# Kernel optimization log

Measured on AMD Instinct MI355X. Metric: run time of the kernel, lower is better.

Reference implementation:

```python
import jax, jax.numpy as jnp
import numpy as np
import math

LOG2PI = math.log(2.0 * math.pi)

def _silu(x):
    return x * jax.nn.sigmoid(x)

def _gru(x, W_ih, W_hh, b_ih, b_hh):
    # x: [B,T,X]; torch nn.GRU single layer, batch_first
    B = x.shape[0]
    H = W_hh.shape[1]
    gi_all = jnp.einsum('btx,gx->btg', x, W_ih) + b_ih  # [B,T,3H] input gates precomputed
    def step(h, gi):
        gh = h @ W_hh.T + b_hh
        i_r, i_z, i_n = jnp.split(gi, 3, axis=-1)
        h_r, h_z, h_n = jnp.split(gh, 3, axis=-1)
        r = jax.nn.sigmoid(i_r + h_r)
        z = jax.nn.sigmoid(i_z + h_z)
        n = jnp.tanh(i_n + r * h_n)
        h_new = (1.0 - z) * n + z * h
        return h_new, h_new
    h0 = jnp.zeros((B, H), x.dtype)
    h_last, h_seq = jax.lax.scan(step, h0, jnp.swapaxes(gi_all, 0, 1))
    return jnp.swapaxes(h_seq, 0, 1), h_last  # [B,T,H], [B,H]

def _A_Q(kappa, sigma, dt):
    A = jnp.exp(-kappa * dt)
    two_k_dt = 2.0 * kappa * dt
    small = (two_k_dt < 1e-6).astype(dt.dtype)
    Q_exact = sigma ** 2 * (1.0 - jnp.exp(-two_k_dt)) / jnp.maximum(2.0 * kappa, 1e-12)
    Q_taylor = sigma ** 2 * dt * (1.0 - kappa * dt + two_k_dt ** 2 / 6.0)
    Q = small * Q_taylor + (1.0 - small) * Q_exact
    return A, Q

def _ou_posterior(m0, s0, mu_k, A_k, Q_k, eps0, eps):
    B, Tm1, C = mu_k.shape
    c0 = m0 + s0 * eps0  # [B,C]
    s0c = jnp.maximum(s0, 1e-12)
    log_q0 = -0.5 * (((c0 - m0) / s0c) ** 2 + 2.0 * jnp.log(s0c) + LOG2PI).sum(-1)
    noise = eps * jnp.sqrt(jnp.maximum(Q_k, 1e-12))
    b = (1.0 - A_k) * mu_k + noise
    Phi_prefix = jnp.cumprod(A_k, axis=1)  # [B,T-1,C]
    Phi_full = jnp.concatenate([jnp.ones((B, 1, C), mu_k.dtype), Phi_prefix], axis=1)
    denom = jnp.maximum(Phi_full[:, 1:, :], 1e-20)
    s = b / denom
    S_full = jnp.concatenate([jnp.zeros((B, 1, C), mu_k.dtype), jnp.cumsum(s, axis=1)], axis=1)
    c = Phi_full * (c0[:, None, :] + S_full)  # [B,T,C]
    mean_trans = mu_k + A_k * (c[:, :-1, :] - mu_k)
    var_trans = jnp.maximum(Q_k, 1e-12)
    log_q_trans = -0.5 * ((c[:, 1:, :] - mean_trans) ** 2 / var_trans + jnp.log(var_trans) + LOG2PI)
    log_q = log_q0 + log_q_trans.sum(-1).sum(-1)
    return c, log_q

def reference(x, t, eps0, eps, W_ih, W_hh, b_ih, b_hh, Wi1, bi1, Wi2, bi2, Ws1, bs1, Ws2, bs2, Ws3, bs3):
    B, T, _ = x.shape
    h_seq, h_global = _gru(x, W_ih, W_hh, b_ih, b_hh)
    # soft time attention, temperature = 1.0
    delta = t[:, :, None, 0] - t[:, None, :, 0]  # [B,T,T]
    logits = -(T * delta) ** 2  # / tau^2 with tau=1
    w = jax.nn.softmax(logits, axis=-1)
    attn = jnp.einsum('bkj,bjh->bkh', w, h_seq)
    # init head
    h0_ctx = h_global + attn[:, 0, :]
    hi = _silu(h0_ctx @ Wi1.T + bi1)
    m0, logs0 = jnp.split(hi @ Wi2.T + bi2, 2, axis=-1)
    s0 = jax.nn.softplus(logs0) + 1e-6
    # step head on ctx[:, :-1]
    ctx = jnp.concatenate([h_global[:, None, :] + attn, t], axis=-1)[:, :-1, :]
    hs = _silu(ctx @ Ws1.T + bs1)
    hs = _silu(hs @ Ws2.T + bs2)
    params = hs @ Ws3.T + bs3
    mu_k, logk_k, logs_k = jnp.split(params, 3, axis=-1)
    kappa_k = jax.nn.softplus(logk_k) + 1e-6
    sigma_k = jax.nn.softplus(logs_k) + 1e-6
    dt = jnp.maximum(t[:, 1:, :] - t[:, :-1, :], 1e-6)
    A_k, Q_k = _A_Q(kappa_k, sigma_k, dt)
    c, log_q = _ou_posterior(m0, s0, mu_k, A_k, Q_k, eps0, eps)
    return c, log_q

def setup_inputs() -> dict:
    B, T, X, H, C = 8, 2048, 64, 256, 32
    key = jax.random.key(0)
    ks = jax.random.split(key, 16)
    def w(k, shape, scale=0.02):
        return (scale * jax.random.normal(k, shape)).astype(jnp.float32)
    x = jax.random.normal(ks[0], (B, T, X), dtype=jnp.float32)
    t = jnp.sort(jax.random.uniform(ks[1], (B, T, 1), dtype=jnp.float32), axis=1)
    eps0 = jax.random.normal(ks[2], (B, C), dtype=jnp.float32)
    eps = jax.random.normal(ks[3], (B, T - 1, C), dtype=jnp.float32)
    return {
        'x': x, 't': t, 'eps0': eps0, 'eps': eps,
        'W_ih': w(ks[4], (3 * H, X)), 'W_hh': w(ks[5], (3 * H, H)),
        'b_ih': jnp.zeros((3 * H,), jnp.float32), 'b_hh': jnp.zeros((3 * H,), jnp.float32),
        'Wi1': w(ks[6], (H, H)), 'bi1': jnp.zeros((H,), jnp.float32),
        'Wi2': w(ks[7], (2 * C, H)), 'bi2': jnp.zeros((2 * C,), jnp.float32),
        'Ws1': w(ks[8], (H, H + 1)), 'bs1': jnp.zeros((H,), jnp.float32),
        'Ws2': w(ks[9], (H, H)), 'bs2': jnp.zeros((H,), jnp.float32),
        'Ws3': w(ks[10], (3 * C, H)), 'bs3': jnp.zeros((3 * C,), jnp.float32),
    }
```

## Files before the change

### kernel.cpp

```cpp
#include <hip/hip_runtime.h>
#include <hip/hip_fp16.h>

#define LOG2PI_F 1.8378770664093453f

typedef float f32x4 __attribute__((ext_vector_type(4)));
typedef unsigned int u32x4 __attribute__((ext_vector_type(4)));

__device__ __forceinline__ unsigned int packh2(float lo, float hi) {
  unsigned int l = (unsigned int)__half_as_ushort(__float2half(lo));
  unsigned int h = (unsigned int)__half_as_ushort(__float2half(hi));
  return (h << 16) | l;
}

__device__ __forceinline__ float sigmoid_f(float x) { return 1.f / (1.f + __expf(-x)); }
__device__ __forceinline__ float silu_f(float x) { return x * sigmoid_f(x); }
__device__ __forceinline__ float softplus_f(float x) {
  return fmaxf(x, 0.f) + log1pf(__expf(-fabsf(x)));
}
__device__ __forceinline__ float tanh_f(float x) {
  float ax = fabsf(x);
  float e = __expf(2.f * ax);
  return copysignf(1.f - 2.f / (e + 1.f), x);
}

__device__ __forceinline__ void tr_piece(const float* in, float* out, int R, int C,
                                         int i) {
  if (i < R * C) {
    int r = i / C, c = i % C;
    out[c * R + r] = in[i];
  }
}

__global__ void prep_kernel(const float* W_ih, const float* Wi1, const float* Wi2,
                            const float* Ws1, const float* Ws2, const float* Ws3,
                            const float* W_hh, float* WT_ih, float* WT1, float* WT2,
                            float* WTs1, float* WTs2, float* WTs3,
                            unsigned int* Wrow) {
  int blk = blockIdx.x;
  int tid = threadIdx.x;
  if (blk < 192) {
    tr_piece(W_ih, WT_ih, 768, 64, blk * 256 + tid);
  } else if (blk < 448) {
    tr_piece(Wi1, WT1, 256, 256, (blk - 192) * 256 + tid);
  } else if (blk < 512) {
    tr_piece(Wi2, WT2, 64, 256, (blk - 448) * 256 + tid);
  } else if (blk < 769) {
    tr_piece(Ws1, WTs1, 256, 257, (blk - 512) * 256 + tid);
  } else if (blk < 1025) {
    tr_piece(Ws2, WTs2, 256, 256, (blk - 769) * 256 + tid);
  } else if (blk < 1121) {
    tr_piece(Ws3, WTs3, 96, 256, (blk - 1025) * 256 + tid);
  } else {
    int i = (blk - 1121) * 256 + tid;
    if (i < 98304) {
      int r = i >> 7, kp = i & 127;
      Wrow[i] = packh2(W_hh[r * 256 + 2 * kp], W_hh[r * 256 + 2 * kp + 1]);
    }
  }
}

__global__ void gi_gemm(const float* __restrict__ x, const float* __restrict__ WT,
                        const float* __restrict__ bih, float* __restrict__ gi) {
  int m0 = blockIdx.x * 8;
  int g = threadIdx.x;
  __shared__ float xs[8][64];
  for (int i = g; i < 512; i += 256) xs[i >> 6][i & 63] = x[m0 * 64 + i];
  __syncthreads();
  float b0 = bih[g], b1 = bih[g + 256], b2 = bih[g + 512];
  float a0[8], a1[8], a2[8];
#pragma unroll
  for (int r = 0; r < 8; r++) { a0[r] = b0; a1[r] = b1; a2[r] = b2; }
  for (int k = 0; k < 64; k++) {
    const float* w = WT + k * 768;
    float w0 = w[g], w1 = w[g + 256], w2 = w[g + 512];
#pragma unroll
    for (int r = 0; r < 8; r++) {
      float xv = xs[r][k];
      a0[r] = fmaf(w0, xv, a0[r]);
      a1[r] = fmaf(w1, xv, a1[r]);
      a2[r] = fmaf(w2, xv, a2[r]);
    }
  }
#pragma unroll
  for (int r = 0; r < 8; r++) {
    float* o = gi + (m0 + r) * 768;
    o[g] = a0[r];
    o[g + 256] = a1[r];
    o[g + 512] = a2[r];
  }
}

__global__ __launch_bounds__(512, 2) void gru_kernel(
    const unsigned int* __restrict__ Wrow,
    const float* __restrict__ gi,
    const float* __restrict__ bhh,
    float* __restrict__ h_seq)
{
  const int b = blockIdx.x;
  const int tid = threadIdx.x;
  const int lane = tid & 63;
  const int wave = tid >> 6;
  const int quad = lane >> 4;
  const int m16 = lane & 15;

  u32x4 afr[6][8];
#pragma unroll
  for (int mt = 0; mt < 6; mt++) {
    int r = wave * 96 + mt * 16 + m16;
    const u32x4* src = (const u32x4*)(Wrow + r * 128);
#pragma unroll
    for (int kt = 0; kt < 8; kt++) afr[mt][kt] = src[kt * 4 + quad];
  }
#pragma unroll
  for (int mt = 0; mt < 6; mt++)
#pragma unroll
    for (int kt = 0; kt < 8; kt++) asm("" : "+a"(afr[mt][kt]));

  __shared__ __align__(16) unsigned int hpk[2][128];
  __shared__ __align__(16) float als[768];
  if (tid < 128) hpk[0][tid] = 0u;

  float brb = 0.f, bzb = 0.f, bnb = 0.f, gr = 0.f, gz = 0.f, gn = 0.f;
  float h = 0.f;
  const float* gib = gi + b * 2048 * 768;
  float* hsb = h_seq + b * 2048 * 256;
  if (tid < 256) {
    brb = bhh[tid];
    bzb = bhh[256 + tid];
    bnb = bhh[512 + tid];
    gr = gib[tid];
    gz = gib[256 + tid];
    gn = gib[512 + tid];
  }
  __syncthreads();

  for (int t = 0; t < 2048; t++) {
    float grn = 0.f, gzn = 0.f, gnn = 0.f;
    if (tid < 256) {
      const float* g3 = gib + min(t + 1, 2047) * 768;
      grn = g3[tid];
      gzn = g3[256 + tid];
      gnn = g3[512 + tid];
    }

    f32x4 c[6];
#pragma unroll
    for (int mt = 0; mt < 6; mt++) c[mt] = (f32x4)0.0f;
    const u32x4* hp = (const u32x4*)hpk[t & 1];
#pragma unroll
    for (int kt = 0; kt < 8; kt++) {
      u32x4 bv = (u32x4)0u;
      if (m16 == 0) bv = hp[kt * 4 + quad];
#pragma unroll
      for (int mt = 0; mt < 6; mt++)
        asm("v_mfma_f32_16x16x32_f16 %0, %1, %2, %0"
            : "+v"(c[mt])
            : "a"(afr[mt][kt]), "v"(bv));
    }
    __builtin_amdgcn_sched_barrier(0);
    asm volatile("s_nop 7\n\ts_nop 7");
    __builtin_amdgcn_sched_barrier(0);

    if (m16 == 0) {
#pragma unroll
      for (int mt = 0; mt < 6; mt++)
        *(f32x4*)(als + wave * 96 + mt * 16 + quad * 4) = c[mt];
    }
    __syncthreads();

    if (tid < 256) {
      float rv = sigmoid_f(als[tid] + brb + gr);
      float zv = sigmoid_f(als[256 + tid] + bzb + gz);
      float nv = tanh_f(gn + rv * (als[512 + tid] + bnb));
      float hn = (1.f - zv) * nv + zv * h;
      h = hn;
      hsb[t * 256 + tid] = hn;
      float other = __shfl_xor(hn, 1);
      if ((tid & 1) == 0) hpk[(t + 1) & 1][tid >> 1] = packh2(hn, other);
    }
    gr = grn;
    gz = gzn;
    gn = gnn;
    __syncthreads();
  }
}

#define AW 80
__global__ void attn_kernel(const float* __restrict__ h_seq, const float* __restrict__ t,
                            float* __restrict__ ctx) {
  const int blk = blockIdx.x;
  const int b = blk >> 7;
  const int k0 = (blk & 127) << 4;
  const int tid = threadIdx.x;

  __shared__ __align__(16) float ewT[176][16];
  __shared__ float ts[176];
  __shared__ float tks[16];
  __shared__ float rden[16];

  const float* tb = t + b * 2048;
  if (tid < 176) {
    int j = k0 - AW + tid;
    ts[tid] = tb[min(max(j, 0), 2047)];
  }
  if (tid < 16) tks[tid] = tb[k0 + tid];
  __syncthreads();

  for (int p = tid; p < 176 * 16; p += 256) {
    int kk = p & 15, jr = p >> 4;
    int j = k0 - AW + jr;
    float d = 2048.f * (tks[kk] - ts[jr]);
    float e = (j >= 0 && j < 2048) ? __expf(-d * d) : 0.f;
    ewT[jr][kk] = e;
  }
  __syncthreads();

  if (tid < 16) {
    float s = 0.f;
    for (int jr = 0; jr < 176; jr++) s += ewT[jr][tid];
    rden[tid] = 1.f / s;
  }
  __syncthreads();

  float acc[16];
#pragma unroll
  for (int kk = 0; kk < 16; kk++) acc[kk] = 0.f;

  const float* hb = h_seq + b * 2048 * 256;
  for (int jr = 0; jr < 176; jr++) {
    int j = min(max(k0 - AW + jr, 0), 2047);
    float hv = hb[j * 256 + tid];
    const float4* e4 = (const float4*)ewT[jr];
    float4 e0 = e4[0], e1 = e4[1], e2 = e4[2], e3 = e4[3];
    acc[0] = fmaf(e0.x, hv, acc[0]);   acc[1] = fmaf(e0.y, hv, acc[1]);
    acc[2] = fmaf(e0.z, hv, acc[2]);   acc[3] = fmaf(e0.w, hv, acc[3]);
    acc[4] = fmaf(e1.x, hv, acc[4]);   acc[5] = fmaf(e1.y, hv, acc[5]);
    acc[6] = fmaf(e1.z, hv, acc[6]);   acc[7] = fmaf(e1.w, hv, acc[7]);
    acc[8] = fmaf(e2.x, hv, acc[8]);   acc[9] = fmaf(e2.y, hv, acc[9]);
    acc[10] = fmaf(e2.z, hv, acc[10]); acc[11] = fmaf(e2.w, hv, acc[11]);
    acc[12] = fmaf(e3.x, hv, acc[12]); acc[13] = fmaf(e3.y, hv, acc[13]);
    acc[14] = fmaf(e3.z, hv, acc[14]); acc[15] = fmaf(e3.w, hv, acc[15]);
  }

  float hg = hb[2047 * 256 + tid];
  float* cb = ctx + (b * 2048 + k0) * 256 + tid;
#pragma unroll
  for (int kk = 0; kk < 16; kk++) cb[kk * 256] = hg + acc[kk] * rden[kk];
}

__global__ void init_head(const float* __restrict__ ctx, const float* __restrict__ WT1,
                          const float* __restrict__ bi1, const float* __restrict__ WT2,
                          const float* __restrict__ bi2, const float* __restrict__ eps0,
                          float* __restrict__ m0s0, float* __restrict__ lq0) {
  int b = blockIdx.x;
  int g = threadIdx.x;
  __shared__ float xs[256], his[256], ms[64], red[32];
  xs[g] = ctx[(b * 2048) * 256 + g];
  __syncthreads();
  float acc = bi1[g];
#pragma unroll 8
  for (int k = 0; k < 256; k++) acc = fmaf(WT1[k * 256 + g], xs[k], acc);
  his[g] = silu_f(acc);
  __syncthreads();
  if (g < 64) {
    float a2 = bi2[g];
#pragma unroll 8
    for (int k = 0; k < 256; k++) a2 = fmaf(WT2[k * 64 + g], his[k], a2);
    float v = (g < 32) ? a2 : (softplus_f(a2) + 1e-6f);
    m0s0[b * 64 + g] = v;
    ms[g] = v;
  }
  __syncthreads();
  if (g < 32) {
    float m = ms[g], s = ms[32 + g];
    float c0 = m + s * eps0[b * 32 + g];
    float sc = fmaxf(s, 1e-12f);
    float z = (c0 - m) / sc;
    red[g] = z * z + 2.f * __logf(sc) + LOG2PI_F;
  }
  __syncthreads();
  if (g == 0) {
    float s = 0.f;
    for (int i = 0; i < 32; i++) s += red[i];
    lq0[b] = -0.5f * s;
  }
}

__global__ __launch_bounds__(256) void head_fused(
    const float* __restrict__ ctx, const float* __restrict__ WTs1,
    const float* __restrict__ bs1, const float* __restrict__ WTs2,
    const float* __restrict__ bs2, const float* __restrict__ WTs3,
    const float* __restrict__ bs3, const float* __restrict__ t,
    const float* __restrict__ eps, float* __restrict__ Aarr,
    float* __restrict__ Darr, float* __restrict__ Larr) {
  int m0 = blockIdx.x * 8;
  int g = threadIdx.x;
  __shared__ __align__(16) float As[8][256];
  __shared__ __align__(16) float Bs[8][256];
  __shared__ float Ps[8][96];
  __shared__ float trow[8];

#pragma unroll
  for (int r = 0; r < 8; r++) As[r][g] = ctx[(m0 + r) * 256 + g];
  if (g < 8) trow[g] = t[m0 + g];
  __syncthreads();

  {
    float b0 = bs1[g];
    float acc[8] = {b0, b0, b0, b0, b0, b0, b0, b0};
    for (int k4 = 0; k4 < 64; k4++) {
      const float* w = WTs1 + (k4 * 4) * 256 + g;
      float w0v = w[0], w1v = w[256], w2v = w[512], w3v = w[768];
#pragma unroll
      for (int r = 0; r < 8; r++) {
        float4 xv = *(const float4*)(&As[r][k4 * 4]);
        acc[r] = fmaf(w0v, xv.x, acc[r]);
        acc[r] = fmaf(w1v, xv.y, acc[r]);
        acc[r] = fmaf(w2v, xv.z, acc[r]);
        acc[r] = fmaf(w3v, xv.w, acc[r]);
      }
    }
    float we = WTs1[256 * 256 + g];
#pragma unroll
    for (int r = 0; r < 8; r++) Bs[r][g] = silu_f(fmaf(trow[r], we, acc[r]));
  }
  __syncthreads();

  {
    float b0 = bs2[g];
    float acc[8] = {b0, b0, b0, b0, b0, b0, b0, b0};
    for (int k4 = 0; k4 < 64; k4++) {
      const float* w = WTs2 + (k4 * 4) * 256 + g;
      float w0v = w[0], w1v = w[256], w2v = w[512], w3v = w[768];
#pragma unroll
      for (int r = 0; r < 8; r++) {
        float4 xv = *(const float4*)(&Bs[r][k4 * 4]);
        acc[r] = fmaf(w0v, xv.x, acc[r]);
        acc[r] = fmaf(w1v, xv.y, acc[r]);
        acc[r] = fmaf(w2v, xv.z, acc[r]);
        acc[r] = fmaf(w3v, xv.w, acc[r]);
      }
    }
#pragma unroll
    for (int r = 0; r < 8; r++) As[r][g] = silu_f(acc[r]);
  }
  __syncthreads();

  if (g < 96) {
    float b0 = bs3[g];
    float acc[8] = {b0, b0, b0, b0, b0, b0, b0, b0};
    for (int k4 = 0; k4 < 64; k4++) {
      const float* w = WTs3 + (k4 * 4) * 96 + g;
      float w0v = w[0], w1v = w[96], w2v = w[192], w3v = w[288];
#pragma unroll
      for (int r = 0; r < 8; r++) {
        float4 xv = *(const float4*)(&As[r][k4 * 4]);
        acc[r] = fmaf(w0v, xv.x, acc[r]);
        acc[r] = fmaf(w1v, xv.y, acc[r]);
        acc[r] = fmaf(w2v, xv.z, acc[r]);
        acc[r] = fmaf(w3v, xv.w, acc[r]);
      }
    }
#pragma unroll
    for (int r = 0; r < 8; r++) Ps[r][g] = acc[r];
  }
  __syncthreads();

  {
    int r = g >> 5, c = g & 31;
    int k = m0 + r;
    int b = k >> 11, kk = k & 2047;
    if (kk < 2047) {
      float mu = Ps[r][c];
      float kap = softplus_f(Ps[r][32 + c]) + 1e-6f;
      float sg = softplus_f(Ps[r][64 + c]) + 1e-6f;
      float dt = fmaxf(t[k + 1] - t[k], 1e-6f);
      float A = __expf(-kap * dt);
      float tkd = 2.f * kap * dt;
      float Qe = sg * sg * (1.f - A * A) / fmaxf(2.f * kap, 1e-12f);
      float kd = kap * dt;
      float Qt = sg * sg * dt * (1.f - kd + tkd * tkd * (1.f / 6.f));
      float var = fmaxf((tkd < 1e-6f) ? Qt : Qe, 1e-12f);
      float e = eps[(b * 2047 + kk) * 32 + c];
      int idx = (b * 2047 + kk) * 32 + c;
      Aarr[idx] = A;
      Darr[idx] = fmaf(mu, 1.f - A, e * sqrtf(var));
      Larr[idx] = e * e + __logf(var) + LOG2PI_F;
    }
  }
}

__global__ __launch_bounds__(1024) void ou_kernel(
    const float* __restrict__ Aarr, const float* __restrict__ Darr,
    const float* __restrict__ Larr, const float* __restrict__ eps0,
    const float* __restrict__ m0s0, const float* __restrict__ lq0,
    float* __restrict__ out) {
  const int b = blockIdx.x;
  const int c = threadIdx.x & 31;
  const int s = threadIdx.x >> 5;
  const int k0 = s * 64;
  const int k1 = min(k0 + 64, 2047);

  __shared__ float Ps[32][33], Ss[32][33], Cs[32][33], lqs[32][33];

  float P = 1.f, S = 0.f, lq = 0.f;
  for (int k = k0; k < k1; k++) {
    int idx = (b * 2047 + k) * 32 + c;
    float A = Aarr[idx];
    float d = Darr[idx];
    S = fmaf(A, S, d);
    P *= A;
    lq += Larr[idx];
  }
  Ps[c][s] = P;
  Ss[c][s] = S;
  lqs[c][s] = lq;
  __syncthreads();

  if (s == 0) {
    float m0v = m0s0[b * 64 + c];
    float s0v = m0s0[b * 64 + 32 + c];
    float cc = fmaf(s0v, eps0[b * 32 + c], m0v);
    out[(b * 2048) * 32 + c] = cc;
    float lqt = 0.f;
    for (int i = 0; i < 32; i++) {
      Cs[c][i] = cc;
      cc = fmaf(Ps[c][i], cc, Ss[c][i]);
      lqt += lqs[c][i];
    }
    for (int off = 16; off >= 1; off >>= 1) lqt += __shfl_down(lqt, off, 32);
    if (c == 0) out[8 * 2048 * 32 + b] = lq0[b] - 0.5f * lqt;
  }
  __syncthreads();

  float cc = Cs[c][s];
  for (int k = k0; k < k1; k++) {
    int idx = (b * 2047 + k) * 32 + c;
    cc = fmaf(Aarr[idx], cc, Darr[idx]);
    out[(b * 2048 + k + 1) * 32 + c] = cc;
  }
}

extern "C" void kernel_launch(void* const* d_in, const int* in_sizes, int n_in,
                              void* d_out, int out_size, void* d_ws, size_t ws_size,
                              hipStream_t stream) {
  (void)in_sizes; (void)n_in; (void)out_size; (void)ws_size;
  const float* x    = (const float*)d_in[0];
  const float* t    = (const float*)d_in[1];
  const float* eps0 = (const float*)d_in[2];
  const float* eps  = (const float*)d_in[3];
  const float* W_ih = (const float*)d_in[4];
  const float* W_hh = (const float*)d_in[5];
  const float* b_ih = (const float*)d_in[6];
  const float* b_hh = (const float*)d_in[7];
  const float* Wi1  = (const float*)d_in[8];
  const float* bi1  = (const float*)d_in[9];
  const float* Wi2  = (const float*)d_in[10];
  const float* bi2  = (const float*)d_in[11];
  const float* Ws1  = (const float*)d_in[12];
  const float* bs1  = (const float*)d_in[13];
  const float* Ws2  = (const float*)d_in[14];
  const float* bs2  = (const float*)d_in[15];
  const float* Ws3  = (const float*)d_in[16];
  const float* bs3  = (const float*)d_in[17];
  float* out = (float*)d_out;
  float* ws = (float*)d_ws;

  float*        WT_ih = ws + 0;
  unsigned int* Wrow  = (unsigned int*)(ws + 49152);
  float*        WT1   = ws + 147456;
  float*        WT2   = ws + 212992;
  float*        WTs1  = ws + 229376;
  float*        WTs2  = ws + 295168;
  float*        WTs3  = ws + 360704;
  float*        m0s0  = ws + 385280;
  float*        lq0   = ws + 385792;
  float*        gi    = ws + 385800;
  float*        h_seq = gi + 12582912;
  float*        ctx   = h_seq + 4194304;
  float*        Aarr = gi;
  float*        Darr = gi + 524032;
  float*        Larr = gi + 1048064;

  prep_kernel<<<1505, 256, 0, stream>>>(W_ih, Wi1, Wi2, Ws1, Ws2, Ws3, W_hh,
                                        WT_ih, WT1, WT2, WTs1, WTs2, WTs3, Wrow);
  gi_gemm<<<2048, 256, 0, stream>>>(x, WT_ih, b_ih, gi);
  gru_kernel<<<8, 512, 0, stream>>>(Wrow, gi, b_hh, h_seq);
  attn_kernel<<<1024, 256, 0, stream>>>(h_seq, t, ctx);
  init_head<<<8, 256, 0, stream>>>(ctx, WT1, bi1, WT2, bi2, eps0, m0s0, lq0);
  head_fused<<<2048, 256, 0, stream>>>(ctx, WTs1, bs1, WTs2, bs2, WTs3, bs3, t, eps,
                                       Aarr, Darr, Larr);
  ou_kernel<<<8, 1024, 0, stream>>>(Aarr, Darr, Larr, eps0, m0s0, lq0, out);
}
```

Before: 3.654 ms.

## Replace GRU recurrent MFMA matvec with per-thread fdot2 dot products

The GRU recurrence now runs one thread per hidden unit in a 256-thread block. Each thread holds its three W_hh rows as packed fp16, the r row in VGPRs and the z and n rows in AGPRs, and computes the three gate dot products with v_dot2 against the fp16 hidden state broadcast from LDS. This removes the MFMA path, the s_nop padding, the LDS round trip of gate results and one __syncthreads per step, which shortens the per-timestep critical path. In exchange each thread runs a 384-long serial FMA chain per step, every lane issues 32 broadcast LDS reads, register pressure is very high, and AGPR values must move to VGPRs before they can be used.

Measured after the change: 3.604 ms. No clear change (-1.4%).

```diff
diff --git a/kernel.cpp b/kernel.cpp
--- a/kernel.cpp
+++ b/kernel.cpp
@@ -5,6 +5,30 @@
 
 typedef float f32x4 __attribute__((ext_vector_type(4)));
 typedef unsigned int u32x4 __attribute__((ext_vector_type(4)));
+
+typedef _Float16 hf2_t __attribute__((ext_vector_type(2)));
+
+#if defined(__has_builtin)
+#  if __has_builtin(__builtin_amdgcn_fdot2)
+#    define USE_FDOT2 1
+#  endif
+#endif
+#ifndef USE_FDOT2
+#  define USE_FDOT2 0
+#endif
+
+__device__ __forceinline__ float fdot2(unsigned int a, unsigned int b, float c) {
+#if USE_FDOT2
+  return __builtin_amdgcn_fdot2(__builtin_bit_cast(hf2_t, a),
+                                __builtin_bit_cast(hf2_t, b), c, false);
+#else
+  __half2 ha = __builtin_bit_cast(__half2, a);
+  __half2 hb = __builtin_bit_cast(__half2, b);
+  float2 fa = __half22float2(ha);
+  float2 fb = __half22float2(hb);
+  return c + fa.x * fb.x + fa.y * fb.y;
+#endif
+}
 
 __device__ __forceinline__ unsigned int packh2(float lo, float hi) {
   unsigned int l = (unsigned int)__half_as_ushort(__float2half(lo));
@@ -90,94 +114,85 @@
   }
 }
 
-__global__ __launch_bounds__(512, 2) void gru_kernel(
+__global__ __launch_bounds__(256, 1) void gru_kernel(
     const unsigned int* __restrict__ Wrow,
     const float* __restrict__ gi,
     const float* __restrict__ bhh,
     float* __restrict__ h_seq)
 {
   const int b = blockIdx.x;
-  const int tid = threadIdx.x;
-  const int lane = tid & 63;
-  const int wave = tid >> 6;
-  const int quad = lane >> 4;
-  const int m16 = lane & 15;
-
-  u32x4 afr[6][8];
-#pragma unroll
-  for (int mt = 0; mt < 6; mt++) {
-    int r = wave * 96 + mt * 16 + m16;
-    const u32x4* src = (const u32x4*)(Wrow + r * 128);
-#pragma unroll
-    for (int kt = 0; kt < 8; kt++) afr[mt][kt] = src[kt * 4 + quad];
-  }
-#pragma unroll
-  for (int mt = 0; mt < 6; mt++)
-#pragma unroll
-    for (int kt = 0; kt < 8; kt++) asm("" : "+a"(afr[mt][kt]));
+  const int d = threadIdx.x;
+
+  u32x4 wr[32];
+  const u32x4* rp = (const u32x4*)(Wrow + d * 128);
+#pragma unroll
+  for (int i = 0; i < 32; i++) wr[i] = rp[i];
+#pragma unroll
+  for (int i = 0; i < 32; i++)
+    asm("" : "+v"(wr[i].x), "+v"(wr[i].y), "+v"(wr[i].z), "+v"(wr[i].w));
+
+  u32x4 wz[32], wn[32];
+  const u32x4* zp = (const u32x4*)(Wrow + (256 + d) * 128);
+  const u32x4* np = (const u32x4*)(Wrow + (512 + d) * 128);
+#pragma unroll
+  for (int i = 0; i < 32; i++) wz[i] = zp[i];
+#pragma unroll
+  for (int i = 0; i < 32; i++) wn[i] = np[i];
+#pragma unroll
+  for (int i = 0; i < 32; i++) asm("" : "+a"(wz[i]));
+#pragma unroll
+  for (int i = 0; i < 32; i++) asm("" : "+a"(wn[i]));
 
   __shared__ __align__(16) unsigned int hpk[2][128];
-  __shared__ __align__(16) float als[768];
-  if (tid < 128) hpk[0][tid] = 0u;
-
-  float brb = 0.f, bzb = 0.f, bnb = 0.f, gr = 0.f, gz = 0.f, gn = 0.f;
+  if (d < 128) hpk[0][d] = 0u;
+
+  const float br = bhh[d], bz = bhh[256 + d], bn = bhh[512 + d];
   float h = 0.f;
   const float* gib = gi + b * 2048 * 768;
   float* hsb = h_seq + b * 2048 * 256;
-  if (tid < 256) {
-    brb = bhh[tid];
-    bzb = bhh[256 + tid];
-    bnb = bhh[512 + tid];
-    gr = gib[tid];
-    gz = gib[256 + tid];
-    gn = gib[512 + tid];
-  }
+  float gr = gib[d], gz = gib[256 + d], gn = gib[512 + d];
   __syncthreads();
 
   for (int t = 0; t < 2048; t++) {
-    float grn = 0.f, gzn = 0.f, gnn = 0.f;
-    if (tid < 256) {
-      const float* g3 = gib + min(t + 1, 2047) * 768;
-      grn = g3[tid];
-      gzn = g3[256 + tid];
-      gnn = g3[512 + tid];
-    }
-
-    f32x4 c[6];
-#pragma unroll
-    for (int mt = 0; mt < 6; mt++) c[mt] = (f32x4)0.0f;
+#pragma unroll
+    for (int i = 0; i < 32; i++) asm("" : "+a"(wz[i]));
+#pragma unroll
+    for (int i = 0; i < 32; i++) asm("" : "+a"(wn[i]));
+
+    const float* g3 = gib + min(t + 1, 2047) * 768;
+    float grn = g3[d];
+    float gzn = g3[256 + d];
+    float gnn = g3[512 + d];
+
     const u32x4* hp = (const u32x4*)hpk[t & 1];
-#pragma unroll
-    for (int kt = 0; kt < 8; kt++) {
-      u32x4 bv = (u32x4)0u;
-      if (m16 == 0) bv = hp[kt * 4 + quad];
-#pragma unroll
-      for (int mt = 0; mt < 6; mt++)
-        asm("v_mfma_f32_16x16x32_f16 %0, %1, %2, %0"
-            : "+v"(c[mt])
-            : "a"(afr[mt][kt]), "v"(bv));
-    }
-    __builtin_amdgcn_sched_barrier(0);
-    asm volatile("s_nop 7\n\ts_nop 7");
-    __builtin_amdgcn_sched_barrier(0);
-
-    if (m16 == 0) {
-#pragma unroll
-      for (int mt = 0; mt < 6; mt++)
-        *(f32x4*)(als + wave * 96 + mt * 16 + quad * 4) = c[mt];
-    }
-    __syncthreads();
-
-    if (tid < 256) {
-      float rv = sigmoid_f(als[tid] + brb + gr);
-      float zv = sigmoid_f(als[256 + tid] + bzb + gz);
-      float nv = tanh_f(gn + rv * (als[512 + tid] + bnb));
-      float hn = (1.f - zv) * nv + zv * h;
-      h = hn;
-      hsb[t * 256 + tid] = hn;
-      float other = __shfl_xor(hn, 1);
-      if ((tid & 1) == 0) hpk[(t + 1) & 1][tid >> 1] = packh2(hn, other);
-    }
+    float ar = 0.f, az = 0.f, an = 0.f;
+#pragma unroll
+    for (int i = 0; i < 32; i++) {
+      u32x4 hv = hp[i];
+      u32x4 z = wz[i];
+      u32x4 n = wn[i];
+      ar = fdot2(wr[i].x, hv.x, ar);
+      ar = fdot2(wr[i].y, hv.y, ar);
+      ar = fdot2(wr[i].z, hv.z, ar);
+      ar = fdot2(wr[i].w, hv.w, ar);
+      az = fdot2(z.x, hv.x, az);
+      az = fdot2(z.y, hv.y, az);
+      az = fdot2(z.z, hv.z, az);
+      az = fdot2(z.w, hv.w, az);
+      an = fdot2(n.x, hv.x, an);
+      an = fdot2(n.y, hv.y, an);
+      an = fdot2(n.z, hv.z, an);
+      an = fdot2(n.w, hv.w, an);
+    }
+
+    float rv = sigmoid_f(gr + ar + br);
+    float zv = sigmoid_f(gz + az + bz);
+    float nv = tanh_f(gn + rv * (an + bn));
+    float hn = (1.f - zv) * nv + zv * h;
+    h = hn;
+    hsb[t * 256 + d] = hn;
+    float other = __shfl_xor(hn, 1);
+    if ((d & 1) == 0) hpk[(t + 1) & 1][d >> 1] = packh2(hn, other);
     gr = grn;
     gz = gzn;
     gn = gnn;
@@ -485,7 +500,7 @@
   prep_kernel<<<1505, 256, 0, stream>>>(W_ih, Wi1, Wi2, Ws1, Ws2, Ws3, W_hh,
                                         WT_ih, WT1, WT2, WTs1, WTs2, WTs3, Wrow);
   gi_gemm<<<2048, 256, 0, stream>>>(x, WT_ih, b_ih, gi);
-  gru_kernel<<<8, 512, 0, stream>>>(Wrow, gi, b_hh, h_seq);
+  gru_kernel<<<8, 256, 0, stream>>>(Wrow, gi, b_hh, h_seq);
   attn_kernel<<<1024, 256, 0, stream>>>(h_seq, t, ctx);
   init_head<<<8, 256, 0, stream>>>(ctx, WT1, bi1, WT2, bi2, eps0, m0s0, lq0);
   head_fused<<<2048, 256, 0, stream>>>(ctx, WTs1, bs1, WTs2, bs2, WTs3, bs3, t, eps,
```
